# Kernel optimization log

Hardware: AMD Instinct MI355X
Metric: run time of the kernel (lower is better)

## Reference

```python
import jax, jax.numpy as jnp
import numpy as np

D_MODEL = 1024
N_HEADS = 8
FF_DIM = 4096
B, T = 4, 2048
LN_EPS = 1e-5


def _layernorm(x, g, b):
    m = jnp.mean(x, axis=-1, keepdims=True)
    v = jnp.mean(jnp.square(x - m), axis=-1, keepdims=True)
    return (x - m) / jnp.sqrt(v + LN_EPS) * g + b


def setup_inputs() -> dict:
    key = jax.random.key(0)
    ks = jax.random.split(key, 16)
    s = 1.0 / np.sqrt(D_MODEL)
    sf = 1.0 / np.sqrt(FF_DIM)
    return {
        "x": jax.random.normal(ks[0], (B, T, D_MODEL), dtype=jnp.float32),
        "wq": jax.random.normal(ks[1], (D_MODEL, D_MODEL), dtype=jnp.float32) * s,
        "bq": jnp.zeros((D_MODEL,), jnp.float32),
        "wk": jax.random.normal(ks[2], (D_MODEL, D_MODEL), dtype=jnp.float32) * s,
        "bk": jnp.zeros((D_MODEL,), jnp.float32),
        "wv": jax.random.normal(ks[3], (D_MODEL, D_MODEL), dtype=jnp.float32) * s,
        "bv": jnp.zeros((D_MODEL,), jnp.float32),
        "wo": jax.random.normal(ks[4], (D_MODEL, D_MODEL), dtype=jnp.float32) * s,
        "bo": jnp.zeros((D_MODEL,), jnp.float32),
        "w1": jax.random.normal(ks[5], (D_MODEL, FF_DIM), dtype=jnp.float32) * s,
        "b1": jnp.zeros((FF_DIM,), jnp.float32),
        "w2": jax.random.normal(ks[6], (FF_DIM, D_MODEL), dtype=jnp.float32) * sf,
        "b2": jnp.zeros((D_MODEL,), jnp.float32),
        "g1": jnp.ones((D_MODEL,), jnp.float32),
        "beta1": jnp.zeros((D_MODEL,), jnp.float32),
        "g2": jnp.ones((D_MODEL,), jnp.float32),
        "beta2": jnp.zeros((D_MODEL,), jnp.float32),
    }


def reference(x, wq, bq, wk, bk, wv, bv, wo, bo, w1, b1, w2, b2, g1, beta1, g2, beta2):
    # NOTE: faithful to the torch module — no head reshape; full-D attention
    # with scale sqrt(D // n_heads).
    scale = np.sqrt(D_MODEL // N_HEADS).astype(np.float32)
    q = x @ wq + bq            # [B,T,D]
    k = x @ wk + bk
    v = x @ wv + bv
    scores = jnp.einsum('btd,bsd->bts', q, k) / scale  # [B,T,T]
    attn = jax.nn.softmax(scores, axis=-1)
    ctx = jnp.einsum('bts,bsd->btd', attn, v)
    x = x + (ctx @ wo + bo)
    x = _layernorm(x, g1, beta1)
    x = x + (jax.nn.relu(x @ w1 + b1) @ w2 + b2)
    x = _layernorm(x, g2, beta2)
    return x
```

## Files before the change

kernel.cpp:

```cpp
#include <hip/hip_runtime.h>
#include <hip/hip_bf16.h>
#include <stdint.h>


typedef __bf16 bf16x8 __attribute__((ext_vector_type(8)));
typedef float f32x4 __attribute__((ext_vector_type(4)));

__device__ __forceinline__ unsigned short f2b(float f) {
    __hip_bfloat16 h = __float2bfloat16(f);
    unsigned short u;
    __builtin_memcpy(&u, &h, 2);
    return u;
}

__device__ __forceinline__ float b2f(unsigned short u) {
    __hip_bfloat16 h;
    __builtin_memcpy(&h, &u, 2);
    return __bfloat162float(h);
}

__device__ __forceinline__ void async_copy16(const unsigned short* g, unsigned short* l) {
    __builtin_amdgcn_global_load_lds((__attribute__((address_space(1))) void*)(g),
                                     (__attribute__((address_space(3))) void*)(l),
                                     16, 0, 0);
}

template <int MODE>
__launch_bounds__(256, 2)
__global__ void gemm_bt(const unsigned short* __restrict__ A, int lda,
                        const unsigned short* __restrict__ Bt, int ldb,
                        void* __restrict__ Cv, int ldc,
                        const float* __restrict__ bias,
                        const unsigned short* __restrict__ resid, int ldr,
                        const float* __restrict__ rowinv,
                        int M, int N, int K,
                        long sA, long sB, long sC, long sR, float scale) {
    constexpr bool OUT_BF16  = (MODE != 3);
    constexpr bool HAS_BIAS  = (MODE == 0 || MODE == 3 || MODE == 4);
    constexpr bool HAS_RESID = (MODE == 3);
    constexpr bool RELU      = (MODE == 4);
    constexpr bool EXPW      = (MODE == 1);
    constexpr bool ROWSCALE  = (MODE == 2);

    __shared__ unsigned short lds_us[16384];
    unsigned short* ldsA = lds_us;
    unsigned short* ldsB = lds_us + 8192;

    const int nx = (int)gridDim.x, ny = (int)gridDim.y;
    int bx, by;
    if ((ny & 7) == 0) {
        const int n     = (int)blockIdx.y * nx + (int)blockIdx.x;
        const int xcd   = n & 7;
        const int slot  = n >> 3;
        const int bandh = ny >> 3;
        by = xcd * bandh + (slot % bandh);
        bx = slot / bandh;
    } else {
        bx = (int)blockIdx.x;
        by = (int)blockIdx.y;
    }

    const int z = blockIdx.z;
    const unsigned short* Ab = A + (long)z * sA + (long)by * 128 * lda;
    const unsigned short* Bb = Bt + (long)z * sB + (long)bx * 128 * ldb;

    const int tid  = threadIdx.x;
    const int lane = tid & 63;
    const int wid  = tid >> 6;
    const int wr   = wid >> 1;
    const int wc   = wid & 1;

    f32x4 acc[4][4] = {};

    long offA[4], offB[4];
    unsigned short* dA[4];
    unsigned short* dB[4];
#pragma unroll
    for (int p = 0; p < 4; ++p) {
        const int s = p * 256 + tid;
        const int r = s >> 3;
        const int c = ((s & 7) ^ (r & 7)) * 8;
        offA[p] = (long)r * lda + c;
        offB[p] = (long)r * ldb + c;
        dA[p] = ldsA + (p * 256 + wid * 64) * 8;
        dB[p] = ldsB + (p * 256 + wid * 64) * 8;
    }

    const int kq = lane >> 4;
    const int rr = lane & 15;
    const int st0 = kq ^ (rr & 7);
    const int st1 = (4 + kq) ^ (rr & 7);

    for (int k0 = 0; k0 < K; k0 += 64) {
        __syncthreads();
#pragma unroll
        for (int p = 0; p < 4; ++p) {
            async_copy16(Ab + offA[p] + k0, dA[p]);
            async_copy16(Bb + offB[p] + k0, dB[p]);
        }
        __syncthreads();

#pragma unroll
        for (int ks = 0; ks < 2; ++ks) {
            const int st = ks ? st1 : st0;
            bf16x8 af[4], bfr[4];
#pragma unroll
            for (int mi = 0; mi < 4; ++mi)
                af[mi] = *(const bf16x8*)(ldsA + (wr * 64 + mi * 16 + rr) * 64 + st * 8);
#pragma unroll
            for (int ni = 0; ni < 4; ++ni)
                bfr[ni] = *(const bf16x8*)(ldsB + (wc * 64 + ni * 16 + rr) * 64 + st * 8);
#pragma unroll
            for (int mi = 0; mi < 4; ++mi)
#pragma unroll
                for (int ni = 0; ni < 4; ++ni)
                    acc[mi][ni] = __builtin_amdgcn_mfma_f32_16x16x32_bf16(af[mi], bfr[ni], acc[mi][ni], 0, 0, 0);
        }
    }

    const long zC = (long)z * sC;
    const int colb = bx * 128 + wc * 64 + rr;
    const int rowb = by * 128 + wr * 64 + kq * 4;
#pragma unroll
    for (int mi = 0; mi < 4; ++mi) {
#pragma unroll
        for (int ni = 0; ni < 4; ++ni) {
            const int col = colb + ni * 16;
            float bv = 0.0f;
            if constexpr (HAS_BIAS) bv = bias[col];
#pragma unroll
            for (int r = 0; r < 4; ++r) {
                const int row = rowb + mi * 16 + r;
                float v = acc[mi][ni][r] * scale + bv;
                if constexpr (EXPW) v = __expf(v - 16.0f);
                if constexpr (ROWSCALE) v *= rowinv[(long)z * sR + row];
                if constexpr (HAS_RESID) v += b2f(resid[(long)z * sR + (long)row * ldr + col]);
                if constexpr (RELU) v = v > 0.0f ? v : 0.0f;
                if constexpr (OUT_BF16)
                    ((unsigned short*)Cv)[zC + (long)row * ldc + col] = f2b(v);
                else
                    ((float*)Cv)[zC + (long)row * ldc + col] = v;
            }
        }
    }
}

__global__ void cast_f32_bf16(const float* __restrict__ in, unsigned short* __restrict__ out, long n) {
    long i = ((long)blockIdx.x * 256 + threadIdx.x) * 4;
    if (i >= n) return;
    float4 v = *(const float4*)(in + i);
    ushort4 o;
    o.x = f2b(v.x); o.y = f2b(v.y); o.z = f2b(v.z); o.w = f2b(v.w);
    *(ushort4*)(out + i) = o;
}

__global__ void concat3(const float* __restrict__ a, const float* __restrict__ b,
                        const float* __restrict__ c, float* __restrict__ o, int n) {
    int i = blockIdx.x * 256 + threadIdx.x;
    if (i < n) { o[i] = a[i]; o[i + n] = b[i]; o[i + 2 * n] = c[i]; }
}

__global__ void transpose_cast(const float* __restrict__ src, unsigned short* __restrict__ dst,
                               int R, int C) {
    __shared__ float tile[32][33];
    const int bx = blockIdx.x * 32;
    const int by = blockIdx.y * 32;
    const int tx = threadIdx.x, ty = threadIdx.y;
#pragma unroll
    for (int i = 0; i < 32; i += 8)
        tile[ty + i][tx] = src[(long)(by + ty + i) * C + bx + tx];
    __syncthreads();
#pragma unroll
    for (int i = 0; i < 32; i += 8)
        dst[(long)(bx + ty + i) * R + by + tx] = f2b(tile[tx][ty + i]);
}

__global__ void transpose_cast4(const float* __restrict__ s0, const float* __restrict__ s1,
                                const float* __restrict__ s2, const float* __restrict__ s3,
                                unsigned short* __restrict__ dst, int N) {
    const float* src = (blockIdx.z == 0) ? s0 : (blockIdx.z == 1) ? s1 : (blockIdx.z == 2) ? s2 : s3;
    unsigned short* d = dst + (long)blockIdx.z * N * N;
    __shared__ float tile[32][33];
    const int bx = blockIdx.x * 32;
    const int by = blockIdx.y * 32;
    const int tx = threadIdx.x, ty = threadIdx.y;
#pragma unroll
    for (int i = 0; i < 32; i += 8)
        tile[ty + i][tx] = src[(long)(by + ty + i) * N + bx + tx];
    __syncthreads();
#pragma unroll
    for (int i = 0; i < 32; i += 8)
        d[(long)(bx + ty + i) * N + by + tx] = f2b(tile[tx][ty + i]);
}

__global__ void transpose_bf16(const unsigned short* __restrict__ src, long sS, int ld,
                               unsigned short* __restrict__ dst, long sD, int R, int C) {
    const int z = blockIdx.z;
    src += (long)z * sS;
    dst += (long)z * sD;
    __shared__ unsigned short tile[32][33];
    const int bx = blockIdx.x * 32;
    const int by = blockIdx.y * 32;
    const int tx = threadIdx.x, ty = threadIdx.y;
#pragma unroll
    for (int i = 0; i < 32; i += 8)
        tile[ty + i][tx] = src[(long)(by + ty + i) * ld + bx + tx];
    __syncthreads();
#pragma unroll
    for (int i = 0; i < 32; i += 8)
        dst[(long)(bx + ty + i) * R + by + tx] = tile[tx][ty + i];
}

__global__ void rowsum_inv(const unsigned short* __restrict__ P, float* __restrict__ inv) {
    const long row = blockIdx.x;
    const ushort4* pr = (const ushort4*)(P + row * 2048);
    const int t = threadIdx.x;
    ushort4 a = pr[t];
    ushort4 b = pr[t + 256];
    float s = b2f(a.x) + b2f(a.y) + b2f(a.z) + b2f(a.w)
            + b2f(b.x) + b2f(b.y) + b2f(b.z) + b2f(b.w);
#pragma unroll
    for (int off = 32; off > 0; off >>= 1) s += __shfl_down(s, off);
    __shared__ float red[4];
    if ((t & 63) == 0) red[t >> 6] = s;
    __syncthreads();
    if (t == 0) inv[row] = 1.0f / (red[0] + red[1] + red[2] + red[3]);
}

template <bool WRITE_F32, bool WRITE_BF16>
__global__ void layernorm_rows(const float* in, float* out, unsigned short* outb,
                               const float* __restrict__ g, const float* __restrict__ b) {
    const long row = blockIdx.x;
    const int t = threadIdx.x;
    const float4 v = ((const float4*)(in + row * 1024))[t];
    float s = v.x + v.y + v.z + v.w;
    float q = v.x * v.x + v.y * v.y + v.z * v.z + v.w * v.w;
#pragma unroll
    for (int off = 32; off > 0; off >>= 1) {
        s += __shfl_down(s, off);
        q += __shfl_down(q, off);
    }
    __shared__ float red[8];
    if ((t & 63) == 0) { red[t >> 6] = s; red[4 + (t >> 6)] = q; }
    __syncthreads();
    s = red[0] + red[1] + red[2] + red[3];
    q = red[4] + red[5] + red[6] + red[7];
    const float mean = s * (1.0f / 1024.0f);
    const float var  = q * (1.0f / 1024.0f) - mean * mean;
    const float inv  = rsqrtf(var + 1e-5f);
    const float4 gg = ((const float4*)g)[t];
    const float4 bb = ((const float4*)b)[t];
    float4 o;
    o.x = (v.x - mean) * inv * gg.x + bb.x;
    o.y = (v.y - mean) * inv * gg.y + bb.y;
    o.z = (v.z - mean) * inv * gg.z + bb.z;
    o.w = (v.w - mean) * inv * gg.w + bb.w;
    if constexpr (WRITE_F32)
        ((float4*)(out + row * 1024))[t] = o;
    if constexpr (WRITE_BF16) {
        ushort4 ob;
        ob.x = f2b(o.x); ob.y = f2b(o.y); ob.z = f2b(o.z); ob.w = f2b(o.w);
        ((ushort4*)(outb + row * 1024))[t] = ob;
    }
}

extern "C" void kernel_launch(void* const* d_in, const int* in_sizes, int n_in,
                              void* d_out, int out_size, void* d_ws, size_t ws_size,
                              hipStream_t stream) {
    (void)in_sizes; (void)n_in; (void)out_size; (void)ws_size;
    const float* x   = (const float*)d_in[0];
    const float* wq  = (const float*)d_in[1];
    const float* bq  = (const float*)d_in[2];
    const float* wk  = (const float*)d_in[3];
    const float* bk  = (const float*)d_in[4];
    const float* wv  = (const float*)d_in[5];
    const float* bv  = (const float*)d_in[6];
    const float* wo  = (const float*)d_in[7];
    const float* bo  = (const float*)d_in[8];
    const float* w1  = (const float*)d_in[9];
    const float* b1  = (const float*)d_in[10];
    const float* w2  = (const float*)d_in[11];
    const float* b2  = (const float*)d_in[12];
    const float* g1  = (const float*)d_in[13];
    const float* be1 = (const float*)d_in[14];
    const float* g2  = (const float*)d_in[15];
    const float* be2 = (const float*)d_in[16];

    const int D = 1024, FF = 4096, T = 2048, M = 8192;
    const size_t MB = 1ull << 20;
    char* w = (char*)d_ws;
    unsigned short* wqT = (unsigned short*)(w + 0 * MB);
    unsigned short* woT = (unsigned short*)(w + 6 * MB);
    unsigned short* w1T = (unsigned short*)(w + 8 * MB);
    unsigned short* w2T = (unsigned short*)(w + 16 * MB);
    unsigned short* xb  = (unsigned short*)(w + 24 * MB);
    unsigned short* qkv = (unsigned short*)(w + 40 * MB);
    float*          rsum = (float*)(w + 40 * MB);
    float*          bcat = (float*)(w + 88 * MB);
    unsigned short* vT  = (unsigned short*)(w + 88 * MB);
    unsigned short* pr  = (unsigned short*)(w + 104 * MB);
    unsigned short* ctxb = (unsigned short*)(w + 136 * MB);
    float*          t0  = (float*)(w + 152 * MB);
    unsigned short* x1b = (unsigned short*)(w + 56 * MB);
    unsigned short* h   = (unsigned short*)(w + 104 * MB);
    float*          y   = (float*)(w + 168 * MB);

    const dim3 tb(32, 8);
    transpose_cast4<<<dim3(32, 32, 4), tb, 0, stream>>>(wq, wk, wv, wo, wqT, D);
    transpose_cast<<<dim3(128, 32), tb, 0, stream>>>(w1, w1T, D, FF);
    transpose_cast<<<dim3(32, 128), tb, 0, stream>>>(w2, w2T, FF, D);
    concat3<<<4, 256, 0, stream>>>(bq, bk, bv, bcat, D);
    cast_f32_bf16<<<8192, 256, 0, stream>>>(x, xb, (long)M * D);

    gemm_bt<0><<<dim3(24, 64, 1), 256, 0, stream>>>(xb, D, wqT, D, qkv, 3 * D, bcat, nullptr, 0,
                                                    nullptr, M, 3 * D, D, 0, 0, 0, 0, 1.0f);

    transpose_bf16<<<dim3(32, 64, 4), tb, 0, stream>>>(qkv + 2 * D, (long)T * 3 * D, 3 * D,
                                                       vT, (long)D * T, T, D);

    gemm_bt<1><<<dim3(16, 16, 4), 256, 0, stream>>>(qkv, 3 * D, qkv + D, 3 * D, pr, T,
                                                    nullptr, nullptr, 0, nullptr, T, T, D,
                                                    (long)T * 3 * D, (long)T * 3 * D, (long)T * T, 0,
                                                    0.08838834764831845f);
    rowsum_inv<<<8192, 256, 0, stream>>>(pr, rsum);

    gemm_bt<2><<<dim3(8, 16, 4), 256, 0, stream>>>(pr, T, vT, T, ctxb, D,
                                                   nullptr, nullptr, 0, rsum, T, D, T,
                                                   (long)T * T, (long)D * T, (long)T * D, T, 1.0f);

    gemm_bt<3><<<dim3(8, 64, 1), 256, 0, stream>>>(ctxb, D, woT, D, t0, D, bo, xb, D,
                                                   nullptr, M, D, D, 0, 0, 0, 0, 1.0f);

    layernorm_rows<false, true><<<8192, 256, 0, stream>>>(t0, nullptr, x1b, g1, be1);

    gemm_bt<4><<<dim3(32, 64, 1), 256, 0, stream>>>(x1b, D, w1T, D, h, FF, b1, nullptr, 0,
                                                    nullptr, M, FF, D, 0, 0, 0, 0, 1.0f);
    gemm_bt<3><<<dim3(8, 64, 1), 256, 0, stream>>>(h, FF, w2T, FF, y, D, b2, x1b, D,
                                                   nullptr, M, D, FF, 0, 0, 0, 0, 1.0f);

    layernorm_rows<true, false><<<8192, 256, 0, stream>>>(y, (float*)d_out, nullptr, g2, be2);
}
```

Before: 476.4 us.

## Load GEMM B fragments directly from global and store residual outputs as bf16

The GEMM kernel no longer stages the B tile through LDS. Each wave reads its B fragments straight from global memory into registers, which halves shared memory use and may allow more resident blocks. The residual GEMM outputs (t0, y) are now written as bf16, and the layernorm kernels read bf16 input, so intermediate traffic is smaller. The trade-offs are uncoalesced, unshared global loads of B, repeated across the two waves that share a column tile, and lower precision in the pre-layernorm sums.

New measurement: 773.5 us. 1.62x slower.

```diff
diff --git a/kernel.cpp b/kernel.cpp
--- a/kernel.cpp
+++ b/kernel.cpp
@@ -29,22 +29,19 @@
 __launch_bounds__(256, 2)
 __global__ void gemm_bt(const unsigned short* __restrict__ A, int lda,
                         const unsigned short* __restrict__ Bt, int ldb,
-                        void* __restrict__ Cv, int ldc,
+                        unsigned short* __restrict__ Cv, int ldc,
                         const float* __restrict__ bias,
                         const unsigned short* __restrict__ resid, int ldr,
                         const float* __restrict__ rowinv,
                         int M, int N, int K,
                         long sA, long sB, long sC, long sR, float scale) {
-    constexpr bool OUT_BF16  = (MODE != 3);
     constexpr bool HAS_BIAS  = (MODE == 0 || MODE == 3 || MODE == 4);
     constexpr bool HAS_RESID = (MODE == 3);
     constexpr bool RELU      = (MODE == 4);
     constexpr bool EXPW      = (MODE == 1);
     constexpr bool ROWSCALE  = (MODE == 2);
 
-    __shared__ unsigned short lds_us[16384];
-    unsigned short* ldsA = lds_us;
-    unsigned short* ldsB = lds_us + 8192;
+    __shared__ unsigned short ldsA[8192];
 
     const int nx = (int)gridDim.x, ny = (int)gridDim.y;
     int bx, by;
@@ -72,18 +69,15 @@
 
     f32x4 acc[4][4] = {};
 
-    long offA[4], offB[4];
+    long offA[4];
     unsigned short* dA[4];
-    unsigned short* dB[4];
 #pragma unroll
     for (int p = 0; p < 4; ++p) {
         const int s = p * 256 + tid;
         const int r = s >> 3;
         const int c = ((s & 7) ^ (r & 7)) * 8;
         offA[p] = (long)r * lda + c;
-        offB[p] = (long)r * ldb + c;
         dA[p] = ldsA + (p * 256 + wid * 64) * 8;
-        dB[p] = ldsB + (p * 256 + wid * 64) * 8;
     }
 
     const int kq = lane >> 4;
@@ -91,30 +85,35 @@
     const int st0 = kq ^ (rr & 7);
     const int st1 = (4 + kq) ^ (rr & 7);
 
+    const unsigned short* Bl[4];
+#pragma unroll
+    for (int ni = 0; ni < 4; ++ni)
+        Bl[ni] = Bb + (long)(wc * 64 + ni * 16 + rr) * ldb + kq * 8;
+
     for (int k0 = 0; k0 < K; k0 += 64) {
         __syncthreads();
 #pragma unroll
-        for (int p = 0; p < 4; ++p) {
-            async_copy16(Ab + offA[p] + k0, dA[p]);
-            async_copy16(Bb + offB[p] + k0, dB[p]);
-        }
+        for (int p = 0; p < 4; ++p) async_copy16(Ab + offA[p] + k0, dA[p]);
+        bf16x8 bre[2][4];
+#pragma unroll
+        for (int ks = 0; ks < 2; ++ks)
+#pragma unroll
+            for (int ni = 0; ni < 4; ++ni)
+                bre[ks][ni] = *(const bf16x8*)(Bl[ni] + k0 + ks * 32);
         __syncthreads();
 
 #pragma unroll
         for (int ks = 0; ks < 2; ++ks) {
             const int st = ks ? st1 : st0;
-            bf16x8 af[4], bfr[4];
+            bf16x8 af[4];
 #pragma unroll
             for (int mi = 0; mi < 4; ++mi)
                 af[mi] = *(const bf16x8*)(ldsA + (wr * 64 + mi * 16 + rr) * 64 + st * 8);
 #pragma unroll
-            for (int ni = 0; ni < 4; ++ni)
-                bfr[ni] = *(const bf16x8*)(ldsB + (wc * 64 + ni * 16 + rr) * 64 + st * 8);
-#pragma unroll
             for (int mi = 0; mi < 4; ++mi)
 #pragma unroll
                 for (int ni = 0; ni < 4; ++ni)
-                    acc[mi][ni] = __builtin_amdgcn_mfma_f32_16x16x32_bf16(af[mi], bfr[ni], acc[mi][ni], 0, 0, 0);
+                    acc[mi][ni] = __builtin_amdgcn_mfma_f32_16x16x32_bf16(af[mi], bre[ks][ni], acc[mi][ni], 0, 0, 0);
         }
     }
 
@@ -136,10 +135,7 @@
                 if constexpr (ROWSCALE) v *= rowinv[(long)z * sR + row];
                 if constexpr (HAS_RESID) v += b2f(resid[(long)z * sR + (long)row * ldr + col]);
                 if constexpr (RELU) v = v > 0.0f ? v : 0.0f;
-                if constexpr (OUT_BF16)
-                    ((unsigned short*)Cv)[zC + (long)row * ldc + col] = f2b(v);
-                else
-                    ((float*)Cv)[zC + (long)row * ldc + col] = v;
+                Cv[zC + (long)row * ldc + col] = f2b(v);
             }
         }
     }
@@ -227,12 +223,15 @@
     if (t == 0) inv[row] = 1.0f / (red[0] + red[1] + red[2] + red[3]);
 }
 
-template <bool WRITE_F32, bool WRITE_BF16>
-__global__ void layernorm_rows(const float* in, float* out, unsigned short* outb,
+template <bool OUT_F32>
+__global__ void layernorm_bf16(const unsigned short* __restrict__ in, float* outf,
+                               unsigned short* outb,
                                const float* __restrict__ g, const float* __restrict__ b) {
     const long row = blockIdx.x;
     const int t = threadIdx.x;
-    const float4 v = ((const float4*)(in + row * 1024))[t];
+    const ushort4 u = ((const ushort4*)(in + row * 1024))[t];
+    float4 v;
+    v.x = b2f(u.x); v.y = b2f(u.y); v.z = b2f(u.z); v.w = b2f(u.w);
     float s = v.x + v.y + v.z + v.w;
     float q = v.x * v.x + v.y * v.y + v.z * v.z + v.w * v.w;
 #pragma unroll
@@ -255,9 +254,9 @@
     o.y = (v.y - mean) * inv * gg.y + bb.y;
     o.z = (v.z - mean) * inv * gg.z + bb.z;
     o.w = (v.w - mean) * inv * gg.w + bb.w;
-    if constexpr (WRITE_F32)
-        ((float4*)(out + row * 1024))[t] = o;
-    if constexpr (WRITE_BF16) {
+    if constexpr (OUT_F32) {
+        ((float4*)(outf + row * 1024))[t] = o;
+    } else {
         ushort4 ob;
         ob.x = f2b(o.x); ob.y = f2b(o.y); ob.z = f2b(o.z); ob.w = f2b(o.w);
         ((ushort4*)(outb + row * 1024))[t] = ob;
@@ -300,10 +299,10 @@
     unsigned short* vT  = (unsigned short*)(w + 88 * MB);
     unsigned short* pr  = (unsigned short*)(w + 104 * MB);
     unsigned short* ctxb = (unsigned short*)(w + 136 * MB);
-    float*          t0  = (float*)(w + 152 * MB);
+    unsigned short* t0  = (unsigned short*)(w + 152 * MB);
     unsigned short* x1b = (unsigned short*)(w + 56 * MB);
-    unsigned short* h   = (unsigned short*)(w + 104 * MB);
-    float*          y   = (float*)(w + 168 * MB);
+    unsigned short* h   = (unsigned short*)(w + 88 * MB);
+    unsigned short* y   = (unsigned short*)(w + 168 * MB);
 
     const dim3 tb(32, 8);
     transpose_cast4<<<dim3(32, 32, 4), tb, 0, stream>>>(wq, wk, wv, wo, wqT, D);
@@ -331,12 +330,12 @@
     gemm_bt<3><<<dim3(8, 64, 1), 256, 0, stream>>>(ctxb, D, woT, D, t0, D, bo, xb, D,
                                                    nullptr, M, D, D, 0, 0, 0, 0, 1.0f);
 
-    layernorm_rows<false, true><<<8192, 256, 0, stream>>>(t0, nullptr, x1b, g1, be1);
+    layernorm_bf16<false><<<8192, 256, 0, stream>>>(t0, nullptr, x1b, g1, be1);
 
     gemm_bt<4><<<dim3(32, 64, 1), 256, 0, stream>>>(x1b, D, w1T, D, h, FF, b1, nullptr, 0,
                                                     nullptr, M, FF, D, 0, 0, 0, 0, 1.0f);
     gemm_bt<3><<<dim3(8, 64, 1), 256, 0, stream>>>(h, FF, w2T, FF, y, D, b2, x1b, D,
                                                    nullptr, M, D, FF, 0, 0, 0, 0, 1.0f);
 
-    layernorm_rows<true, false><<<8192, 256, 0, stream>>>(y, (float*)d_out, nullptr, g2, be2);
-}
+    layernorm_bf16<true><<<8192, 256, 0, stream>>>(y, (float*)d_out, nullptr, g2, be2);
+}
```
